# Optimization experiments

Measured on AMD Instinct MI355X. Metric: run time of the kernel, lower is better.

## Reference

```python
import jax, jax.numpy as jnp
import numpy as np

N = 50000   # total nodes
D = 128     # feature dim
E = 800000  # edges (avg degree 16)
G = 100     # graphs (500 nodes each)


def setup_inputs() -> dict:
    key = jax.random.key(0)
    ks = jax.random.split(key, 9)
    s = 1.0 / np.sqrt(D)
    X = jax.random.normal(ks[0], (N, D), jnp.float32)
    src = jax.random.randint(ks[1], (E,), 0, N)
    dst = jax.random.randint(ks[2], (E,), 0, N)
    edge_index = jnp.stack([src, dst])  # [2, E]
    edge_weight = jax.random.uniform(ks[3], (E,), jnp.float32)
    # 100 graphs of 500 nodes each (graph_sizes = [500]*100)
    segment_ids = jnp.repeat(jnp.arange(G), N // G)
    return {
        "X": X,
        "edge_weight": edge_weight,
        "W1": jax.random.normal(ks[4], (D, D), jnp.float32) * s,
        "b1": jnp.zeros((D,), jnp.float32),
        "W2": jax.random.normal(ks[5], (D, D), jnp.float32) * s,
        "b2": jnp.zeros((D,), jnp.float32),
        "Wf": jax.random.normal(ks[6], (D, 1), jnp.float32) * s,
        "bf": jnp.zeros((1,), jnp.float32),
        "edge_index": edge_index,
        "segment_ids": segment_ids,
    }


def gcn_conv(X, edge_index, edge_weight, W, b):
    # h_v = sum_{(u->v)} w_e * (X @ W)[u] + b   (sparse A @ XW)
    h = X @ W                                   # [N, d_out]
    msgs = h[edge_index[0]] * edge_weight[:, None]  # [E, d_out]
    agg = jax.ops.segment_sum(msgs, edge_index[1], num_segments=N)
    return agg + b


def reference(X, edge_weight, W1, b1, W2, b2, Wf, bf, edge_index, segment_ids):
    # layer stack: conv -> relu -> dropout(eval=identity)
    h = jax.nn.relu(gcn_conv(X, edge_index, edge_weight, W1, b1))
    h = jax.nn.relu(gcn_conv(h, edge_index, edge_weight, W2, b2))
    out = jax.nn.sigmoid(gcn_conv(h, edge_index, edge_weight, Wf, bf))  # [N, 1]
    # fused per-graph mean readout (replaces split(graph_sizes) python loop)
    sums = jax.ops.segment_sum(out.sum(axis=1), segment_ids, num_segments=G)
    counts = jax.ops.segment_sum(jnp.ones((N,), out.dtype), segment_ids, num_segments=G)
    return sums / (counts * out.shape[1])  # [G]
```

## Files before the change

kernel.cpp:

```cpp
#include <hip/hip_runtime.h>
#include <hip/hip_fp16.h>

#define N_NODES 50000
#define DIM 128
#define NEDGE 800000
#define NGRAPH 100
#define NPG 500
#define NBUCKET 250
#define NPB 200
#define BCAP 4096
#define CHUNK 2048
#define EPT (CHUNK / 256)

typedef _Float16 f16x8 __attribute__((ext_vector_type(8)));
typedef float f32x4 __attribute__((ext_vector_type(4)));
typedef float f32x2 __attribute__((ext_vector_type(2)));

__device__ inline float wgt(unsigned p) {
    return __half2float(__ushort_as_half((unsigned short)(p & 0xffffu)));
}
__device__ inline void accrow(uint2 q, float w, float* acc) {
    f32x2 f;
    f = __builtin_amdgcn_cvt_pk_f32_fp8((int)q.x, false); acc[0] = fmaf(w, f[0], acc[0]); acc[1] = fmaf(w, f[1], acc[1]);
    f = __builtin_amdgcn_cvt_pk_f32_fp8((int)q.x, true);  acc[2] = fmaf(w, f[0], acc[2]); acc[3] = fmaf(w, f[1], acc[3]);
    f = __builtin_amdgcn_cvt_pk_f32_fp8((int)q.y, false); acc[4] = fmaf(w, f[0], acc[4]); acc[5] = fmaf(w, f[1], acc[5]);
    f = __builtin_amdgcn_cvt_pk_f32_fp8((int)q.y, true);  acc[6] = fmaf(w, f[0], acc[6]); acc[7] = fmaf(w, f[1], acc[7]);
}
__device__ inline unsigned pack_fp8x4(float a, float b, float c, float d) {
    int v = __builtin_amdgcn_cvt_pk_fp8_f32(a, b, 0, false);
    v = __builtin_amdgcn_cvt_pk_fp8_f32(c, d, v, true);
    return (unsigned)v;
}

__global__ void prep(const float* __restrict__ W1, const float* __restrict__ W2,
                     _Float16* __restrict__ fragW1, _Float16* __restrict__ fragW2,
                     int* __restrict__ gCur) {
    const int b = blockIdx.x;
    if (b == 128) {
        int t = threadIdx.x;
        if (t < NBUCKET) gCur[t] = t * BCAP;
        return;
    }
    const float* W = (b < 64) ? W1 : W2;
    _Float16* F = (b < 64) ? fragW1 : fragW2;
    int idx = (b & 63) * 256 + threadIdx.x;
    int j = idx & 7, l = (idx >> 3) & 63, kt = (idx >> 9) & 3, nt = idx >> 11;
    int k = kt * 32 + ((l >> 4) << 3) + j;
    int col = (nt << 4) + (l & 15);
    F[idx] = (_Float16)W[k * DIM + col];
}

__global__ void bucket_scatter(const int* __restrict__ src, const int* __restrict__ dst,
                               const float* __restrict__ w, int* __restrict__ gCur,
                               uint2* __restrict__ stage, int E) {
    __shared__ int hist[NBUCKET];
    __shared__ int base[NBUCKET];
    for (int i = threadIdx.x; i < NBUCKET; i += 256) hist[i] = 0;
    __syncthreads();
    const int e0 = blockIdx.x * CHUNK;
    int myDst[EPT];
#pragma unroll
    for (int j = 0; j < EPT; ++j) {
        int e = e0 + j * 256 + threadIdx.x;
        int d = (e < E) ? dst[e] : -1;
        myDst[j] = d;
        if (d >= 0) atomicAdd(&hist[d / NPB], 1);
    }
    __syncthreads();
    for (int i = threadIdx.x; i < NBUCKET; i += 256)
        base[i] = atomicAdd(&gCur[i], hist[i]);
    __syncthreads();
#pragma unroll
    for (int j = 0; j < EPT; ++j) {
        int d = myDst[j];
        if (d >= 0) {
            int e = e0 + j * 256 + threadIdx.x;
            int b = d / NPB;
            int p = atomicAdd(&base[b], 1);
            unsigned short wh = __half_as_ushort(__float2half_rn(w[e]));
            stage[p] = make_uint2(((unsigned)src[e] << 16) | (unsigned)wh,
                                  (unsigned)(d - b * NPB));
        }
    }
}

__global__ void bucket_build(const int* __restrict__ gCur, const uint2* __restrict__ stage,
                             unsigned int* __restrict__ pack, int2* __restrict__ range) {
    __shared__ int lhist[NPB];
    __shared__ int lincl[256];
    __shared__ int lcur[NPB];
    const int b = blockIdx.x;
    const int t = threadIdx.x;
    const int cnt = gCur[b] - b * BCAP;
    for (int i = t; i < NPB; i += 256) lhist[i] = 0;
    __syncthreads();
    unsigned myX[BCAP / 256];
    int myLd[BCAP / 256];
#pragma unroll
    for (int j = 0; j < BCAP / 256; ++j) {
        int i = j * 256 + t;
        if (i < cnt) {
            uint2 r = stage[b * BCAP + i];
            myX[j] = r.x;
            myLd[j] = (int)r.y;
            atomicAdd(&lhist[r.y], 1);
        } else {
            myLd[j] = -1;
        }
    }
    __syncthreads();
    int h = (t < NPB) ? lhist[t] : 0;
    lincl[t] = h;
    __syncthreads();
    for (int off = 1; off < 256; off <<= 1) {
        int v = (t >= off) ? lincl[t - off] : 0;
        __syncthreads();
        lincl[t] += v;
        __syncthreads();
    }
    if (t < NPB) lcur[t] = lincl[t] - h;
    __syncthreads();
#pragma unroll
    for (int j = 0; j < BCAP / 256; ++j) {
        if (myLd[j] >= 0) {
            int p = atomicAdd(&lcur[myLd[j]], 1);
            pack[b * BCAP + p] = myX[j];
        }
    }
    if (t < NPB) {
        int v = b * NPB + t;
        range[v] = make_int2(b * BCAP + lincl[t] - h, b * BCAP + lincl[t]);
    }
}

__device__ inline f16x8 load_afrag_f32(const float* a) {
    float4 u0 = *(const float4*)a;
    float4 u1 = *(const float4*)(a + 4);
    f16x8 r;
    r[0] = (_Float16)u0.x; r[1] = (_Float16)u0.y; r[2] = (_Float16)u0.z; r[3] = (_Float16)u0.w;
    r[4] = (_Float16)u1.x; r[5] = (_Float16)u1.y; r[6] = (_Float16)u1.z; r[7] = (_Float16)u1.w;
    return r;
}
__device__ inline f16x8 load_afrag_fp8(const unsigned char* a) {
    uint2 q = *(const uint2*)a;
    f32x2 f0 = __builtin_amdgcn_cvt_pk_f32_fp8((int)q.x, false);
    f32x2 f1 = __builtin_amdgcn_cvt_pk_f32_fp8((int)q.x, true);
    f32x2 f2 = __builtin_amdgcn_cvt_pk_f32_fp8((int)q.y, false);
    f32x2 f3 = __builtin_amdgcn_cvt_pk_f32_fp8((int)q.y, true);
    f16x8 r;
    r[0] = (_Float16)f0[0]; r[1] = (_Float16)f0[1]; r[2] = (_Float16)f1[0]; r[3] = (_Float16)f1[1];
    r[4] = (_Float16)f2[0]; r[5] = (_Float16)f2[1]; r[6] = (_Float16)f3[0]; r[7] = (_Float16)f3[1];
    return r;
}

template <typename TIN>
__global__ __launch_bounds__(512) void gemm_mfma(const TIN* __restrict__ A,
                                                 const _Float16* __restrict__ fragWg,
                                                 unsigned char* __restrict__ C) {
    __shared__ __align__(16) _Float16 fragW[16384];
    const int tid = threadIdx.x;
    for (int i = tid; i < 2048; i += 512)
        ((uint4*)fragW)[i] = ((const uint4*)fragWg)[i];
    __syncthreads();
    const int lane = tid & 63;
    const int wid = tid >> 6;
    const int row0 = blockIdx.x * 128 + wid * 16;
    if (row0 >= N_NODES) return;
    const int arow = row0 + (lane & 15);
    const int koff = (lane >> 4) << 3;
    f32x4 acc[8] = {};
#pragma unroll
    for (int kt = 0; kt < 4; ++kt) {
        f16x8 a;
        const TIN* ap = A + (size_t)arow * DIM + kt * 32 + koff;
        if constexpr (sizeof(TIN) == 4) a = load_afrag_f32((const float*)ap);
        else                            a = load_afrag_fp8((const unsigned char*)ap);
#pragma unroll
        for (int nt = 0; nt < 8; ++nt) {
            f16x8 b = *(const f16x8*)&fragW[(((nt << 2) | kt) << 9) | (lane << 3)];
            acc[nt] = __builtin_amdgcn_mfma_f32_16x16x32_f16(a, b, acc[nt], 0, 0, 0);
        }
    }
    const int crow = row0 + ((lane >> 4) << 2);
    const int ccol = lane & 15;
#pragma unroll
    for (int nt = 0; nt < 8; ++nt) {
#pragma unroll
        for (int r = 0; r < 4; ++r) {
            int v8 = __builtin_amdgcn_cvt_pk_fp8_f32(acc[nt][r], acc[nt][r], 0, false);
            C[(size_t)(crow + r) * DIM + (nt << 4) + ccol] = (unsigned char)(v8 & 0xff);
        }
    }
}

template <int MODE>
__global__ void gather_feat(const unsigned char* __restrict__ msg,
                            const unsigned int* __restrict__ pack,
                            const int2* __restrict__ range, const float* __restrict__ bias,
                            const float* __restrict__ wf, unsigned char* __restrict__ outF,
                            float* __restrict__ outS) {
    int gid = blockIdx.x * blockDim.x + threadIdx.x;
    int grp = gid >> 4, lane = gid & 15;
    if (grp >= N_NODES) return;
    int2 r = range[grp];
    int beg = r.x, end = r.y;
    float acc[8] = {};
    int i = beg;
    for (; i + 3 < end; i += 4) {
        unsigned p0 = pack[i], p1 = pack[i + 1], p2 = pack[i + 2], p3 = pack[i + 3];
        uint2 q0 = ((const uint2*)(msg + (size_t)(p0 >> 16) * DIM))[lane];
        uint2 q1 = ((const uint2*)(msg + (size_t)(p1 >> 16) * DIM))[lane];
        uint2 q2 = ((const uint2*)(msg + (size_t)(p2 >> 16) * DIM))[lane];
        uint2 q3 = ((const uint2*)(msg + (size_t)(p3 >> 16) * DIM))[lane];
        accrow(q0, wgt(p0), acc);
        accrow(q1, wgt(p1), acc);
        accrow(q2, wgt(p2), acc);
        accrow(q3, wgt(p3), acc);
    }
    for (; i < end; ++i) {
        unsigned p = pack[i];
        uint2 q = ((const uint2*)(msg + (size_t)(p >> 16) * DIM))[lane];
        accrow(q, wgt(p), acc);
    }
    float4 b0 = ((const float4*)bias)[2 * lane];
    float4 b1 = ((const float4*)bias)[2 * lane + 1];
    acc[0] = fmaxf(acc[0] + b0.x, 0.f); acc[1] = fmaxf(acc[1] + b0.y, 0.f);
    acc[2] = fmaxf(acc[2] + b0.z, 0.f); acc[3] = fmaxf(acc[3] + b0.w, 0.f);
    acc[4] = fmaxf(acc[4] + b1.x, 0.f); acc[5] = fmaxf(acc[5] + b1.y, 0.f);
    acc[6] = fmaxf(acc[6] + b1.z, 0.f); acc[7] = fmaxf(acc[7] + b1.w, 0.f);
    if (MODE == 0) {
        uint2 o;
        o.x = pack_fp8x4(acc[0], acc[1], acc[2], acc[3]);
        o.y = pack_fp8x4(acc[4], acc[5], acc[6], acc[7]);
        ((uint2*)(outF + (size_t)grp * DIM))[lane] = o;
    } else {
        float4 f0 = ((const float4*)wf)[2 * lane];
        float4 f1 = ((const float4*)wf)[2 * lane + 1];
        float d = acc[0] * f0.x + acc[1] * f0.y + acc[2] * f0.z + acc[3] * f0.w
                + acc[4] * f1.x + acc[5] * f1.y + acc[6] * f1.z + acc[7] * f1.w;
#pragma unroll
        for (int off = 8; off; off >>= 1) d += __shfl_down(d, off, 16);
        if (lane == 0) outS[grp] = d;
    }
}

__global__ void final_readout(const float* __restrict__ s, const unsigned int* __restrict__ pack,
                              const int2* __restrict__ range, const float* __restrict__ bfp,
                              float* __restrict__ out) {
    __shared__ float red[256];
    int g = blockIdx.x;
    float bf = bfp[0];
    float sum = 0.f;
    for (int n = threadIdx.x; n < NPG; n += blockDim.x) {
        int v = g * NPG + n;
        int2 r = range[v];
        float a = 0.f;
        for (int i = r.x; i < r.y; ++i) {
            unsigned int p = pack[i];
            a += wgt(p) * s[p >> 16];
        }
        a += bf;
        sum += 1.f / (1.f + expf(-a));
    }
    red[threadIdx.x] = sum;
    __syncthreads();
    for (int t = 128; t > 0; t >>= 1) {
        if (threadIdx.x < t) red[threadIdx.x] += red[threadIdx.x + t];
        __syncthreads();
    }
    if (threadIdx.x == 0) out[g] = red[0] / (float)NPG;
}

extern "C" void kernel_launch(void* const* d_in, const int* in_sizes, int n_in,
                              void* d_out, int out_size, void* d_ws, size_t ws_size,
                              hipStream_t stream) {
    const float* X  = (const float*)d_in[0];
    const float* ew = (const float*)d_in[1];
    const float* W1 = (const float*)d_in[2];
    const float* b1 = (const float*)d_in[3];
    const float* W2 = (const float*)d_in[4];
    const float* b2 = (const float*)d_in[5];
    const float* Wf = (const float*)d_in[6];
    const float* bf = (const float*)d_in[7];
    const int* ei   = (const int*)d_in[8];
    const int* src  = ei;
    const int* dst  = ei + NEDGE;

    float* out = (float*)d_out;

    char* ws = (char*)d_ws;
    size_t off = 0;
    unsigned char* bufA = (unsigned char*)(ws + off); off += (size_t)N_NODES * DIM;
    unsigned char* bufB = (unsigned char*)(ws + off); off += (size_t)N_NODES * DIM;
    uint2* stage = (uint2*)(ws + off);  off += (size_t)NBUCKET * BCAP * 8;
    unsigned int* pack = (unsigned int*)(ws + off); off += (size_t)NBUCKET * BCAP * 4;
    int2* range = (int2*)(ws + off);    off += (size_t)N_NODES * 8;
    int* gCur   = (int*)(ws + off);     off += (size_t)256 * 4;
    _Float16* fragW1 = (_Float16*)(ws + off); off += (size_t)16384 * 2;
    _Float16* fragW2 = (_Float16*)(ws + off); off += (size_t)16384 * 2;
    float* s_node = (float*)(ws + off); off += (size_t)N_NODES * 4;

    const int TB = 256;
    const int SCAT_BLK = (NEDGE + CHUNK - 1) / CHUNK;
    const int GATHER_BLK = (N_NODES * 16 + TB - 1) / TB;
    const int MFMA_BLK = (N_NODES + 127) / 128;

    prep<<<129, TB, 0, stream>>>(W1, W2, fragW1, fragW2, gCur);
    bucket_scatter<<<SCAT_BLK, TB, 0, stream>>>(src, dst, ew, gCur, stage, NEDGE);
    bucket_build<<<NBUCKET, TB, 0, stream>>>(gCur, stage, pack, range);

    gemm_mfma<float><<<MFMA_BLK, 512, 0, stream>>>(X, fragW1, bufA);
    gather_feat<0><<<GATHER_BLK, TB, 0, stream>>>(bufA, pack, range, b1,
                                                  nullptr, bufB, nullptr);
    gemm_mfma<unsigned char><<<MFMA_BLK, 512, 0, stream>>>(bufB, fragW2, bufA);
    gather_feat<1><<<GATHER_BLK, TB, 0, stream>>>(bufA, pack, range, b2,
                                                  Wf, nullptr, s_node);
    final_readout<<<NGRAPH, TB, 0, stream>>>(s_node, pack, range, bf, out);
}
```

Measured before the change: 112.9 us.

## Fuse first GEMM with bucket build into one launch; deepen gather unroll

```diff
diff --git a/kernel.cpp b/kernel.cpp
--- a/kernel.cpp
+++ b/kernel.cpp
@@ -84,55 +84,6 @@
     }
 }
 
-__global__ void bucket_build(const int* __restrict__ gCur, const uint2* __restrict__ stage,
-                             unsigned int* __restrict__ pack, int2* __restrict__ range) {
-    __shared__ int lhist[NPB];
-    __shared__ int lincl[256];
-    __shared__ int lcur[NPB];
-    const int b = blockIdx.x;
-    const int t = threadIdx.x;
-    const int cnt = gCur[b] - b * BCAP;
-    for (int i = t; i < NPB; i += 256) lhist[i] = 0;
-    __syncthreads();
-    unsigned myX[BCAP / 256];
-    int myLd[BCAP / 256];
-#pragma unroll
-    for (int j = 0; j < BCAP / 256; ++j) {
-        int i = j * 256 + t;
-        if (i < cnt) {
-            uint2 r = stage[b * BCAP + i];
-            myX[j] = r.x;
-            myLd[j] = (int)r.y;
-            atomicAdd(&lhist[r.y], 1);
-        } else {
-            myLd[j] = -1;
-        }
-    }
-    __syncthreads();
-    int h = (t < NPB) ? lhist[t] : 0;
-    lincl[t] = h;
-    __syncthreads();
-    for (int off = 1; off < 256; off <<= 1) {
-        int v = (t >= off) ? lincl[t - off] : 0;
-        __syncthreads();
-        lincl[t] += v;
-        __syncthreads();
-    }
-    if (t < NPB) lcur[t] = lincl[t] - h;
-    __syncthreads();
-#pragma unroll
-    for (int j = 0; j < BCAP / 256; ++j) {
-        if (myLd[j] >= 0) {
-            int p = atomicAdd(&lcur[myLd[j]], 1);
-            pack[b * BCAP + p] = myX[j];
-        }
-    }
-    if (t < NPB) {
-        int v = b * NPB + t;
-        range[v] = make_int2(b * BCAP + lincl[t] - h, b * BCAP + lincl[t]);
-    }
-}
-
 __device__ inline f16x8 load_afrag_f32(const float* a) {
     float4 u0 = *(const float4*)a;
     float4 u1 = *(const float4*)(a + 4);
@@ -154,6 +105,40 @@
 }
 
 template <typename TIN>
+__device__ inline void gemm_tile(const TIN* __restrict__ A, const _Float16* fragW,
+                                 unsigned char* __restrict__ C, int blk, int tid) {
+    const int lane = tid & 63;
+    const int wid = tid >> 6;
+    const int row0 = blk * 128 + wid * 16;
+    if (row0 >= N_NODES) return;
+    const int arow = row0 + (lane & 15);
+    const int koff = (lane >> 4) << 3;
+    f32x4 acc[8] = {};
+#pragma unroll
+    for (int kt = 0; kt < 4; ++kt) {
+        f16x8 a;
+        const TIN* ap = A + (size_t)arow * DIM + kt * 32 + koff;
+        if constexpr (sizeof(TIN) == 4) a = load_afrag_f32((const float*)ap);
+        else                            a = load_afrag_fp8((const unsigned char*)ap);
+#pragma unroll
+        for (int nt = 0; nt < 8; ++nt) {
+            f16x8 b = *(const f16x8*)&fragW[(((nt << 2) | kt) << 9) | (lane << 3)];
+            acc[nt] = __builtin_amdgcn_mfma_f32_16x16x32_f16(a, b, acc[nt], 0, 0, 0);
+        }
+    }
+    const int crow = row0 + ((lane >> 4) << 2);
+    const int ccol = lane & 15;
+#pragma unroll
+    for (int nt = 0; nt < 8; ++nt) {
+#pragma unroll
+        for (int r = 0; r < 4; ++r) {
+            int v8 = __builtin_amdgcn_cvt_pk_fp8_f32(acc[nt][r], acc[nt][r], 0, false);
+            C[(size_t)(crow + r) * DIM + (nt << 4) + ccol] = (unsigned char)(v8 & 0xff);
+        }
+    }
+}
+
+template <typename TIN>
 __global__ __launch_bounds__(512) void gemm_mfma(const TIN* __restrict__ A,
                                                  const _Float16* __restrict__ fragWg,
                                                  unsigned char* __restrict__ C) {
@@ -162,34 +147,68 @@
     for (int i = tid; i < 2048; i += 512)
         ((uint4*)fragW)[i] = ((const uint4*)fragWg)[i];
     __syncthreads();
-    const int lane = tid & 63;
-    const int wid = tid >> 6;
-    const int row0 = blockIdx.x * 128 + wid * 16;
-    if (row0 >= N_NODES) return;
-    const int arow = row0 + (lane & 15);
-    const int koff = (lane >> 4) << 3;
-    f32x4 acc[8] = {};
-#pragma unroll
-    for (int kt = 0; kt < 4; ++kt) {
-        f16x8 a;
-        const TIN* ap = A + (size_t)arow * DIM + kt * 32 + koff;
-        if constexpr (sizeof(TIN) == 4) a = load_afrag_f32((const float*)ap);
-        else                            a = load_afrag_fp8((const unsigned char*)ap);
-#pragma unroll
-        for (int nt = 0; nt < 8; ++nt) {
-            f16x8 b = *(const f16x8*)&fragW[(((nt << 2) | kt) << 9) | (lane << 3)];
-            acc[nt] = __builtin_amdgcn_mfma_f32_16x16x32_f16(a, b, acc[nt], 0, 0, 0);
-        }
-    }
-    const int crow = row0 + ((lane >> 4) << 2);
-    const int ccol = lane & 15;
-#pragma unroll
-    for (int nt = 0; nt < 8; ++nt) {
-#pragma unroll
-        for (int r = 0; r < 4; ++r) {
-            int v8 = __builtin_amdgcn_cvt_pk_fp8_f32(acc[nt][r], acc[nt][r], 0, false);
-            C[(size_t)(crow + r) * DIM + (nt << 4) + ccol] = (unsigned char)(v8 & 0xff);
-        }
+    gemm_tile<TIN>(A, fragW, C, blockIdx.x, tid);
+}
+
+#define MFMA_BLK ((N_NODES + 127) / 128)
+__global__ __launch_bounds__(512) void gemm1_build(
+        const float* __restrict__ A, const _Float16* __restrict__ fragWg,
+        unsigned char* __restrict__ C, const int* __restrict__ gCur,
+        const uint2* __restrict__ stage, unsigned int* __restrict__ pack,
+        int2* __restrict__ range) {
+    __shared__ __align__(16) _Float16 fragW[16384];
+    __shared__ int lhist[NPB];
+    __shared__ int lincl[256];
+    __shared__ int lcur[NPB];
+    const int tid = threadIdx.x;
+    if (blockIdx.x < MFMA_BLK) {
+        for (int i = tid; i < 2048; i += 512)
+            ((uint4*)fragW)[i] = ((const uint4*)fragWg)[i];
+        __syncthreads();
+        gemm_tile<float>(A, fragW, C, blockIdx.x, tid);
+        return;
+    }
+    const int b = blockIdx.x - MFMA_BLK;
+    const int t = tid;
+    const int cnt = gCur[b] - b * BCAP;
+    for (int i = t; i < NPB; i += 512) lhist[i] = 0;
+    __syncthreads();
+    unsigned myX[BCAP / 512];
+    int myLd[BCAP / 512];
+#pragma unroll
+    for (int j = 0; j < BCAP / 512; ++j) {
+        int i = j * 512 + t;
+        if (i < cnt) {
+            uint2 r = stage[b * BCAP + i];
+            myX[j] = r.x;
+            myLd[j] = (int)r.y;
+            atomicAdd(&lhist[r.y], 1);
+        } else {
+            myLd[j] = -1;
+        }
+    }
+    __syncthreads();
+    int h = (t < NPB) ? lhist[t] : 0;
+    if (t < 256) lincl[t] = h;
+    __syncthreads();
+    for (int off = 1; off < 256; off <<= 1) {
+        int v = (t >= off && t < 256) ? lincl[t - off] : 0;
+        __syncthreads();
+        if (t < 256) lincl[t] += v;
+        __syncthreads();
+    }
+    if (t < NPB) lcur[t] = lincl[t] - h;
+    __syncthreads();
+#pragma unroll
+    for (int j = 0; j < BCAP / 512; ++j) {
+        if (myLd[j] >= 0) {
+            int p = atomicAdd(&lcur[myLd[j]], 1);
+            pack[b * BCAP + p] = myX[j];
+        }
+    }
+    if (t < NPB) {
+        int v = b * NPB + t;
+        range[v] = make_int2(b * BCAP + lincl[t] - h, b * BCAP + lincl[t]);
     }
 }
 
@@ -206,6 +225,17 @@
     int beg = r.x, end = r.y;
     float acc[8] = {};
     int i = beg;
+    for (; i + 7 < end; i += 8) {
+        unsigned p[8];
+        uint2 q[8];
+#pragma unroll
+        for (int j = 0; j < 8; ++j) p[j] = pack[i + j];
+#pragma unroll
+        for (int j = 0; j < 8; ++j)
+            q[j] = ((const uint2*)(msg + (size_t)(p[j] >> 16) * DIM))[lane];
+#pragma unroll
+        for (int j = 0; j < 8; ++j) accrow(q[j], wgt(p[j]), acc);
+    }
     for (; i + 3 < end; i += 4) {
         unsigned p0 = pack[i], p1 = pack[i + 1], p2 = pack[i + 2], p3 = pack[i + 3];
         uint2 q0 = ((const uint2*)(msg + (size_t)(p0 >> 16) * DIM))[lane];
@@ -303,13 +333,11 @@
     const int TB = 256;
     const int SCAT_BLK = (NEDGE + CHUNK - 1) / CHUNK;
     const int GATHER_BLK = (N_NODES * 16 + TB - 1) / TB;
-    const int MFMA_BLK = (N_NODES + 127) / 128;
 
     prep<<<129, TB, 0, stream>>>(W1, W2, fragW1, fragW2, gCur);
     bucket_scatter<<<SCAT_BLK, TB, 0, stream>>>(src, dst, ew, gCur, stage, NEDGE);
-    bucket_build<<<NBUCKET, TB, 0, stream>>>(gCur, stage, pack, range);
-
-    gemm_mfma<float><<<MFMA_BLK, 512, 0, stream>>>(X, fragW1, bufA);
+    gemm1_build<<<MFMA_BLK + NBUCKET, 512, 0, stream>>>(X, fragW1, bufA, gCur,
+                                                        stage, pack, range);
     gather_feat<0><<<GATHER_BLK, TB, 0, stream>>>(bufA, pack, range, b1,
                                                   nullptr, bufB, nullptr);
     gemm_mfma<unsigned char><<<MFMA_BLK, 512, 0, stream>>>(bufB, fragW2, bufA);
```

Measured after the change: 106.9 us. 5.3% less time.
